# Kernel optimization log

Hardware: AMD Instinct MI355X
Metric: run time of the kernel (lower is better)

## Reference

```python
import jax, jax.numpy as jnp
from jax import lax
import numpy as np

N, T, PD, TD, F, E, GB = 2048, 256, 5, 5, 128, 65536, 5


def _lstm_layer(x, Wih, Whh, bih, bhh):
    # x: [B, T, D] -> [B, T, H], torch LSTM gate order (i, f, g, o)
    B = x.shape[0]
    H = Whh.shape[1]
    b = bih + bhh

    def step(carry, xt):
        h, c = carry
        gates = xt @ Wih.T + h @ Whh.T + b
        i, f, g, o = jnp.split(gates, 4, axis=-1)
        c = jax.nn.sigmoid(f) * c + jax.nn.sigmoid(i) * jnp.tanh(g)
        h = jax.nn.sigmoid(o) * jnp.tanh(c)
        return (h, c), h

    h0 = jnp.zeros((B, H), x.dtype)
    _, hs = lax.scan(step, (h0, h0), jnp.swapaxes(x, 0, 1))
    return jnp.swapaxes(hs, 0, 1)


def _attention(x, W1, b1, W2, b2):
    # Fused prefix (cumulative causal) softmax attention.
    # Original loops over t computing softmax(scores[:, :t+1]); here:
    # ctx[t] = cumsum(e * x)[t] / cumsum(e)[t] with a global max shift
    # (softmax is shift-invariant, so this equals the per-prefix softmax).
    s = (jnp.tanh(x @ W1.T + b1) @ W2.T + b2)[..., 0]  # [B, T]
    e = jnp.exp(s - jnp.max(s, axis=1, keepdims=True))  # [B, T]
    num = jnp.cumsum(e[..., None] * x, axis=1)          # [B, T, D]
    den = jnp.cumsum(e, axis=1)[..., None]              # [B, T, 1]
    return jnp.sum(num / den, axis=1)                   # [B, D]


def _gcn(x, W, b, edge_index, edge_weight):
    # PyG GCNConv with normalize=True: add self-loops (w=1), symmetric norm.
    n = x.shape[0]
    loop = jnp.arange(n)
    row = jnp.concatenate([edge_index[0], loop])
    col = jnp.concatenate([edge_index[1], loop])
    w = jnp.concatenate([edge_weight, jnp.ones((n,), edge_weight.dtype)])
    deg = jax.ops.segment_sum(w, col, num_segments=n)
    dinv = jnp.where(deg > 0, deg ** -0.5, 0.0)
    norm = dinv[row] * w * dinv[col]
    h = x @ W.T
    out = jax.ops.segment_sum(norm[:, None] * h[row], col, num_segments=n)
    return out + b


def _forward(price, global_trend, p_weights, t_weights,
             lp_Wih0, lp_Whh0, lp_bih0, lp_bhh0, lp_Wih1, lp_Whh1, lp_bih1, lp_bhh1,
             lt_Wih0, lt_Whh0, lt_bih0, lt_bhh0, lt_Wih1, lt_Whh1, lt_bih1, lt_bhh1,
             ap_W1, ap_b1, ap_W2, ap_b2, at_W1, at_b1, at_W2, at_b2,
             gp1_W, gp1_b, gp2_W, gp2_b, gt1_W, gt1_b, gt2_W, gt2_b,
             mlp_W, mlp_b, p_edge_index, t_edge_index):
    x = _lstm_layer(price, lp_Wih0, lp_Whh0, lp_bih0, lp_bhh0)
    x = _lstm_layer(x, lp_Wih1, lp_Whh1, lp_bih1, lp_bhh1)
    x = _attention(x, ap_W1, ap_b1, ap_W2, ap_b2)            # [N, F]
    g = _lstm_layer(global_trend, lt_Wih0, lt_Whh0, lt_bih0, lt_bhh0)
    g = _lstm_layer(g, lt_Wih1, lt_Whh1, lt_bih1, lt_bhh1)
    g = _attention(g, at_W1, at_b1, at_W2, at_b2)            # [GB, F]
    pg = _gcn(x, gp1_W, gp1_b, p_edge_index, p_weights)
    pg = _gcn(pg, gp2_W, gp2_b, p_edge_index, p_weights)     # [N, F]
    # NOTE: original feeds x (not g) into the trend graph convs.
    tg = _gcn(x, gt1_W, gt1_b, t_edge_index, t_weights)
    tg = _gcn(tg, gt2_W, gt2_b, t_edge_index, t_weights)     # [N, F]
    trend = tg @ g.T                                         # [N, GB]
    feat = jnp.concatenate([pg, trend], axis=1)              # [N, F+GB]
    return jax.nn.sigmoid(feat @ mlp_W.T + mlp_b)            # [N, 1]


def setup_inputs() -> dict:
    key = jax.random.key(0)
    ks = iter(jax.random.split(key, 64))
    nrm = lambda shape, s=0.05: jax.random.normal(next(ks), shape, jnp.float32) * s
    inp = {}
    inp['price'] = jax.random.normal(next(ks), (N, T, PD), jnp.float32)
    inp['global_trend'] = jax.random.normal(next(ks), (GB, T, TD), jnp.float32)
    inp['p_edge_index'] = jax.random.randint(next(ks), (2, E), 0, N)
    inp['p_weights'] = jax.random.uniform(next(ks), (E,), jnp.float32)
    inp['t_edge_index'] = jax.random.randint(next(ks), (2, E), 0, N)
    inp['t_weights'] = jax.random.uniform(next(ks), (E,), jnp.float32)
    for pre, d in (('lp', PD), ('lt', TD)):
        inp[pre + '_Wih0'] = nrm((4 * F, d)); inp[pre + '_Whh0'] = nrm((4 * F, F))
        inp[pre + '_bih0'] = nrm((4 * F,));   inp[pre + '_bhh0'] = nrm((4 * F,))
        inp[pre + '_Wih1'] = nrm((4 * F, F)); inp[pre + '_Whh1'] = nrm((4 * F, F))
        inp[pre + '_bih1'] = nrm((4 * F,));   inp[pre + '_bhh1'] = nrm((4 * F,))
    for pre in ('ap', 'at'):
        inp[pre + '_W1'] = nrm((F, F)); inp[pre + '_b1'] = jnp.zeros((F,), jnp.float32)
        inp[pre + '_W2'] = nrm((1, F)); inp[pre + '_b2'] = jnp.zeros((1,), jnp.float32)
    for pre in ('gp', 'gt'):
        inp[pre + '1_W'] = nrm((16, F)); inp[pre + '1_b'] = jnp.zeros((16,), jnp.float32)
        inp[pre + '2_W'] = nrm((F, 16)); inp[pre + '2_b'] = jnp.zeros((F,), jnp.float32)
    inp['mlp_W'] = nrm((1, F + GB)); inp['mlp_b'] = jnp.zeros((1,), jnp.float32)
    return inp


def reference(price, global_trend, p_edge_index, p_weights, t_edge_index, t_weights,
              lp_Wih0, lp_Whh0, lp_bih0, lp_bhh0, lp_Wih1, lp_Whh1, lp_bih1, lp_bhh1,
              lt_Wih0, lt_Whh0, lt_bih0, lt_bhh0, lt_Wih1, lt_Whh1, lt_bih1, lt_bhh1,
              ap_W1, ap_b1, ap_W2, ap_b2, at_W1, at_b1, at_W2, at_b2,
              gp1_W, gp1_b, gp2_W, gp2_b, gt1_W, gt1_b, gt2_W, gt2_b,
              mlp_W, mlp_b):
    return _forward(price, global_trend, p_weights, t_weights,
                    lp_Wih0, lp_Whh0, lp_bih0, lp_bhh0, lp_Wih1, lp_Whh1, lp_bih1, lp_bhh1,
                    lt_Wih0, lt_Whh0, lt_bih0, lt_bhh0, lt_Wih1, lt_Whh1, lt_bih1, lt_bhh1,
                    ap_W1, ap_b1, ap_W2, ap_b2, at_W1, at_b1, at_W2, at_b2,
                    gp1_W, gp1_b, gp2_W, gp2_b, gt1_W, gt1_b, gt2_W, gt2_b,
                    mlp_W, mlp_b, p_edge_index, t_edge_index)
```

## Files before the change

### kernel.cpp

```cpp
#include <hip/hip_runtime.h>
#include <hip/hip_bf16.h>
#include <cstddef>

#define TT    256
#define NROW  2048
#define GBN   5
#define EDG   65536

using f32x4  = __attribute__((ext_vector_type(4))) float;
using bf16x8 = __attribute__((ext_vector_type(8))) short;

__device__ __forceinline__ void pinv(bf16x8& x) { asm volatile("" : "+v"(x)); }

__device__ __forceinline__ void barrier_lgkm() {
  asm volatile("s_waitcnt lgkmcnt(0)" ::: "memory");
  __builtin_amdgcn_s_barrier();
}

__device__ __forceinline__ float exp2fa(float x) { float r; asm("v_exp_f32 %0, %1" : "=v"(r) : "v"(x)); return r; }
__device__ __forceinline__ float rcpfa(float x)  { float r; asm("v_rcp_f32 %0, %1" : "=v"(r) : "v"(x)); return r; }
#define L2E 1.4426950408889634f
__device__ __forceinline__ float sigf(float x) { return rcpfa(1.0f + exp2fa(x * -L2E)); }
__device__ __forceinline__ float tanh_fast(float x) {
  float t = exp2fa(x * (-2.0f * L2E));
  return (1.0f - t) * rcpfa(1.0f + t);
}

enum : int {
  XBUF   = 425984,
  GBUFO  = 688128,
  DINVP  = 688768,
  DINVT  = 690816,
  H16    = 692864,
  PG1    = 725632,
  H128   = 758400,
  PGB    = 1020544,
  TG1    = 1282688,
  TGB    = 1315456,
  WS_END = 1577600
};

enum : int {
  N_P0   = 0,
  N_P1I  = 65536,
  N_P1H  = 131072,
  N_PA   = 196608,
  N_T0   = 212992,
  N_T1I  = 278528,
  N_T1H  = 344064,
  N_TA   = 409600
};

enum : long long {
  C0S_O   = 1577600,
  C1S_O   = 1841792,
  H1IMG_O = 2105984,
  SMST_O  = 2370176,
  NUMS_O  = 2374304,
  ACCOS_O = 2638496,
  H0S_O   = 2902688
};

struct SmemPipe {
  ushort a[2][2048];
  ushort b[2][2048];
  float  x[2560];
  float  s[2][8][16];
};

__global__ void k_pack(const float* __restrict__ Wa, const float* __restrict__ Wb,
                       int K1, int K2, int NT, int KS, ushort* __restrict__ dst) {
  int t = blockIdx.x * blockDim.x + threadIdx.x;
  int total = KS * NT * 2 * 64;
  if (t >= total) return;
  int lane = t & 63;
  int part = (t >> 6) & 1;
  int rest = t >> 7;
  int nt = rest % NT, kk = rest / NT;
  int j = nt * 16 + (lane & 15);
  int kbase = kk * 32 + (lane >> 4) * 8;
  bf16x8 o;
  #pragma unroll
  for (int e = 0; e < 8; ++e) {
    int k = kbase + e;
    float x = (k < K1) ? Wa[(size_t)j * K1 + k] : Wb[(size_t)j * K2 + (k - K1)];
    __hip_bfloat16 hi = __float2bfloat16(x);
    ushort u;
    if (part == 0) {
      u = *(ushort*)&hi;
    } else {
      float lo = x - __bfloat162float(hi);
      __hip_bfloat16 lob = __float2bfloat16(lo);
      u = *(ushort*)&lob;
    }
    o[e] = (short)u;
  }
  ((bf16x8*)dst)[t] = o;
}

__global__ void k_zero(float* __restrict__ p, int n) {
  int i = blockIdx.x * blockDim.x + threadIdx.x;
  if (i < n) p[i] = 0.0f;
}
__global__ void k_fill1(float* __restrict__ p, int n) {
  int i = blockIdx.x * blockDim.x + threadIdx.x;
  if (i < n) p[i] = 1.0f;
}
__global__ void k_deg(const int* __restrict__ col, const float* __restrict__ w,
                      float* __restrict__ deg, int n) {
  int i = blockIdx.x * blockDim.x + threadIdx.x;
  if (i < n) atomicAdd(&deg[col[i]], w[i]);
}
__global__ void k_dinv(float* __restrict__ deg, int n) {
  int i = blockIdx.x * blockDim.x + threadIdx.x;
  if (i < n) deg[i] = rsqrtf(deg[i]);
}

__device__ static void lstm0_body(
    SmemPipe* sm, int b,
    const float* __restrict__ price, const float* __restrict__ gtrend,
    const float* __restrict__ ws_ro, ushort* __restrict__ h0S, float* __restrict__ c0S,
    const float* __restrict__ Wih0p, const float* __restrict__ bi0p, const float* __restrict__ bh0p,
    const float* __restrict__ Wih0t, const float* __restrict__ bi0t, const float* __restrict__ bh0t,
    int nPrice, int t0, int TCp, int first)
{
  const int tid = threadIdx.x;
  const int w = tid >> 6, l = tid & 63;
  const int lq = l >> 4, lr = l & 15;
  const int rb = lq * 4;
  const int kcol = w * 16 + lr;
  const bool isP = b < nPrice;
  const int R = isP ? 16 : GBN;
  const float* seq = isP ? (price + (size_t)b * 16 * (TT * 5)) : gtrend;
  const ushort* S0 = (const ushort*)(ws_ro + (isP ? N_P0 : N_T0));
  const float* Wih0 = isP ? Wih0p : Wih0t;
  const float* bi0 = isP ? bi0p : bi0t;
  const float* bh0 = isP ? bh0p : bh0t;

  auto h0hi = sm->a;
  auto h0lo = sm->b;
  float* xsa = sm->x;

  bf16x8 wh[4][4], wl[4][4];
  #pragma unroll
  for (int kk = 0; kk < 4; ++kk)
    #pragma unroll
    for (int g = 0; g < 4; ++g) {
      int blk = (kk * 32 + (w + 8 * g)) * 2;
      wh[kk][g] = ((const bf16x8*)S0)[(blk + 0) * 64 + l];
      wl[kk][g] = ((const bf16x8*)S0)[(blk + 1) * 64 + l];
      pinv(wh[kk][g]); pinv(wl[kk][g]);
    }
  float wih0r[4][5], bg0[4];
  #pragma unroll
  for (int g = 0; g < 4; ++g) {
    int j = kcol + 128 * g;
    bg0[g] = bi0[j] + bh0[j];
    #pragma unroll
    for (int k = 0; k < 5; ++k) wih0r[g][k] = Wih0[j * 5 + k];
  }

  const size_t bstr = (size_t)b * (size_t)TCp * 4096;
  float c0[4] = {0, 0, 0, 0};

  for (int i = tid; i < TCp * 80; i += 512) {
    int tl = i / 80, rem = i % 80, r = rem / 5, k = rem % 5;
    xsa[tl * 80 + rem] = (r < R) ? seq[(size_t)r * (TT * 5) + (size_t)(t0 + tl) * 5 + k] : 0.0f;
  }
  if (first) {
    for (int i = tid; i < 2048; i += 512) { h0hi[0][i] = 0; h0lo[0][i] = 0; }
  } else {
    const size_t lb = bstr + (size_t)(TCp - 1) * 4096;
    *(uint2*)&h0hi[0][4 * tid] = *(const uint2*)&h0S[lb + 4 * tid];
    *(uint2*)&h0lo[0][4 * tid] = *(const uint2*)&h0S[lb + 2048 + 4 * tid];
    #pragma unroll
    for (int reg = 0; reg < 4; ++reg)
      c0[reg] = c0S[(size_t)b * 2048 + (size_t)(rb + reg) * 128 + kcol];
  }
  __syncthreads();

  const int kkhi = (kcol >> 3) & 3;
  const int eo = kcol & 7;
  const int b0w = rb + 16 * kkhi;
  const int kkw = kcol >> 5;
  int wro[4];
  #pragma unroll
  for (int reg = 0; reg < 4; ++reg) wro[reg] = kkw * 512 + (b0w + (reg ^ lq)) * 8 + eo;
  const int rdo = (l ^ ((l >> 2) & 3)) * 8;

  int cur = 0;
  for (int tl = 0; tl < TCp; ++tl) {
    const int nxt = cur ^ 1;
    if (tl > 0) {
      *(uint2*)&h0S[bstr + (size_t)(tl - 1) * 4096 + 4 * tid] = *(const uint2*)&h0hi[cur][4 * tid];
      *(uint2*)&h0S[bstr + (size_t)(tl - 1) * 4096 + 2048 + 4 * tid] = *(const uint2*)&h0lo[cur][4 * tid];
    }

    f32x4 acc[4];
    #pragma unroll
    for (int g = 0; g < 4; ++g) acc[g] = (f32x4){bg0[g], bg0[g], bg0[g], bg0[g]};
    #pragma unroll
    for (int k = 0; k < 5; ++k) {
      float xv[4];
      #pragma unroll
      for (int reg = 0; reg < 4; ++reg) xv[reg] = xsa[tl * 80 + (rb + reg) * 5 + k];
      #pragma unroll
      for (int g = 0; g < 4; ++g)
        #pragma unroll
        for (int reg = 0; reg < 4; ++reg)
          acc[g][reg] = fmaf(xv[reg], wih0r[g][k], acc[g][reg]);
    }
    #pragma unroll
    for (int kk = 0; kk < 4; ++kk) {
      bf16x8 ah = *(const bf16x8*)&h0hi[cur][kk * 512 + rdo];
      bf16x8 al = *(const bf16x8*)&h0lo[cur][kk * 512 + rdo];
      #pragma unroll
      for (int g = 0; g < 4; ++g) {
        acc[g] = __builtin_amdgcn_mfma_f32_16x16x32_bf16(ah, wh[kk][g], acc[g], 0, 0, 0);
        acc[g] = __builtin_amdgcn_mfma_f32_16x16x32_bf16(al, wh[kk][g], acc[g], 0, 0, 0);
        acc[g] = __builtin_amdgcn_mfma_f32_16x16x32_bf16(ah, wl[kk][g], acc[g], 0, 0, 0);
      }
    }
    #pragma unroll
    for (int reg = 0; reg < 4; ++reg) {
      float gi = acc[0][reg], gf = acc[1][reg], gg = acc[2][reg], go = acc[3][reg];
      float c = sigf(gf) * c0[reg] + sigf(gi) * tanh_fast(gg);
      c0[reg] = c;
      float h = sigf(go) * tanh_fast(c);
      __hip_bfloat16 hb = __float2bfloat16(h);
      float lo = h - __bfloat162float(hb);
      __hip_bfloat16 lb = __float2bfloat16(lo);
      h0hi[nxt][wro[reg]] = *(ushort*)&hb;
      h0lo[nxt][wro[reg]] = *(ushort*)&lb;
    }
    barrier_lgkm();
    cur = nxt;
  }
  *(uint2*)&h0S[bstr + (size_t)(TCp - 1) * 4096 + 4 * tid] = *(const uint2*)&h0hi[cur][4 * tid];
  *(uint2*)&h0S[bstr + (size_t)(TCp - 1) * 4096 + 2048 + 4 * tid] = *(const uint2*)&h0lo[cur][4 * tid];

  #pragma unroll
  for (int reg = 0; reg < 4; ++reg)
    c0S[(size_t)b * 2048 + (size_t)(rb + reg) * 128 + kcol] = c0[reg];
}

__device__ static void lstm1_body(
    SmemPipe* sm, int b,
    const float* __restrict__ pre1, const float* __restrict__ ws_ro,
    float* __restrict__ xout, float* __restrict__ gout,
    float* __restrict__ c1S, ushort* __restrict__ h1imgS, float* __restrict__ smS,
    float* __restrict__ numS, float* __restrict__ accOS,
    const float* __restrict__ apB1, const float* __restrict__ apW2, const float* __restrict__ apB2,
    const float* __restrict__ atB1, const float* __restrict__ atW2, const float* __restrict__ atB2,
    int nPrice, int TCp, int first)
{
  const int tid = threadIdx.x;
  const int w = tid >> 6, l = tid & 63;
  const int lq = l >> 4, lr = l & 15;
  const int rb = lq * 4;
  const int kcol = w * 16 + lr;
  const bool isP = b < nPrice;
  const int R = isP ? 16 : GBN;
  const ushort* S1H = (const ushort*)(ws_ro + (isP ? N_P1H : N_T1H));
  const ushort* SA  = (const ushort*)(ws_ro + (isP ? N_PA : N_TA));
  const float* b1ap = isP ? apB1 : atB1;
  const float* w2p  = isP ? apW2 : atW2;
  const float  b2v  = isP ? apB2[0] : atB2[0];

  auto h1hi = sm->a;
  auto h1lo = sm->b;
  auto sbuf = sm->s;

  bf16x8 hh[4][4], hl[4][4];
  #pragma unroll
  for (int kk = 0; kk < 4; ++kk)
    #pragma unroll
    for (int g = 0; g < 4; ++g) {
      int blk = (kk * 32 + (w + 8 * g)) * 2;
      hh[kk][g] = ((const bf16x8*)S1H)[(blk + 0) * 64 + l];
      hl[kk][g] = ((const bf16x8*)S1H)[(blk + 1) * 64 + l];
      pinv(hh[kk][g]); pinv(hl[kk][g]);
    }
  bf16x8 wa[4], wal[4];
  #pragma unroll
  for (int kk = 0; kk < 4; ++kk) {
    wa[kk]  = ((const bf16x8*)SA)[((kk * 8 + w) * 2 + 0) * 64 + l];
    wal[kk] = ((const bf16x8*)SA)[((kk * 8 + w) * 2 + 1) * 64 + l];
    pinv(wa[kk]); pinv(wal[kk]);
  }
  const float w2r = w2p[kcol], b1ar = b1ap[kcol];

  float c1[4] = {0, 0, 0, 0}, h1r[4] = {0, 0, 0, 0}, h1r_prev[4];
  float num[4] = {0, 0, 0, 0}, accO[4] = {0, 0, 0, 0};
  float m_run[4], den_r[4];

  if (first) {
    for (int i = tid; i < 2048; i += 512) { h1hi[0][i] = 0; h1lo[0][i] = 0; }
    #pragma unroll
    for (int reg = 0; reg < 4; ++reg) { m_run[reg] = -1e30f; den_r[reg] = 0.0f; }
  } else {
    const size_t ib = (size_t)b * 4096;
    *(uint2*)&h1hi[0][4 * tid] = *(const uint2*)&h1imgS[ib + 4 * tid];
    *(uint2*)&h1lo[0][4 * tid] = *(const uint2*)&h1imgS[ib + 2048 + 4 * tid];
    const size_t sb = (size_t)b * 2048;
    #pragma unroll
    for (int reg = 0; reg < 4; ++reg) {
      size_t o = sb + (size_t)(rb + reg) * 128 + kcol;
      c1[reg] = c1S[o];
      num[reg] = numS[o];
      accO[reg] = accOS[o];
      m_run[reg] = smS[(size_t)b * 32 + (size_t)(rb + reg) * 2];
      den_r[reg] = smS[(size_t)b * 32 + (size_t)(rb + reg) * 2 + 1];
    }
  }
  __syncthreads();

  const int kkhi = (kcol >> 3) & 3;
  const int eo = kcol & 7;
  const int b0w = rb + 16 * kkhi;
  const int kkw = kcol >> 5;
  int wro[4];
  #pragma unroll
  for (int reg = 0; reg < 4; ++reg) wro[reg] = kkw * 512 + (b0w + (reg ^ lq)) * 8 + eo;
  const int rdo = (l ^ ((l >> 2) & 3)) * 8;

  const float* pbase = pre1 + (size_t)b * TCp * 8192 + (size_t)tid * 16;

  f32x4 pnext[4];
  #pragma unroll
  for (int g = 0; g < 4; ++g) pnext[g] = *(const f32x4*)&pbase[g * 4];

  int cur = 0;
  for (int tl = 0; tl < TCp; ++tl) {
    const int nxt = cur ^ 1;
    f32x4 acc[4];
    #pragma unroll
    for (int g = 0; g < 4; ++g) acc[g] = pnext[g];
    if (tl + 1 < TCp) {
      #pragma unroll
      for (int g = 0; g < 4; ++g)
        pnext[g] = *(const f32x4*)&pbase[(size_t)(tl + 1) * 8192 + g * 4];
    }

    #pragma unroll
    for (int kk = 0; kk < 4; ++kk) {
      bf16x8 ah = *(const bf16x8*)&h1hi[cur][kk * 512 + rdo];
      bf16x8 al = *(const bf16x8*)&h1lo[cur][kk * 512 + rdo];
      #pragma unroll
      for (int g = 0; g < 4; ++g) {
        acc[g] = __builtin_amdgcn_mfma_f32_16x16x32_bf16(ah, hh[kk][g], acc[g], 0, 0, 0);
        acc[g] = __builtin_amdgcn_mfma_f32_16x16x32_bf16(al, hh[kk][g], acc[g], 0, 0, 0);
        acc[g] = __builtin_amdgcn_mfma_f32_16x16x32_bf16(ah, hl[kk][g], acc[g], 0, 0, 0);
      }
    }
    #pragma unroll
    for (int reg = 0; reg < 4; ++reg) {
      h1r_prev[reg] = h1r[reg];
      float gi = acc[0][reg], gf = acc[1][reg], gg = acc[2][reg], go = acc[3][reg];
      float c = sigf(gf) * c1[reg] + sigf(gi) * tanh_fast(gg);
      c1[reg] = c;
      float h = sigf(go) * tanh_fast(c);
      h1r[reg] = h;
      __hip_bfloat16 hb = __float2bfloat16(h);
      float lo = h - __bfloat162float(hb);
      __hip_bfloat16 lb = __float2bfloat16(lo);
      h1hi[nxt][wro[reg]] = *(ushort*)&hb;
      h1lo[nxt][wro[reg]] = *(ushort*)&lb;
    }
    barrier_lgkm();

    if (tl > 0) {
      const int pb = (tl - 1) & 1;
      #pragma unroll
      for (int reg = 0; reg < 4; ++reg) {
        float s = b2v;
        #pragma unroll
        for (int ww = 0; ww < 8; ++ww) s += sbuf[pb][ww][rb + reg];
        float m0 = m_run[reg];
        float nm = fmaxf(m0, s);
        float e = exp2fa((s - nm) * L2E), sc = exp2fa((m0 - nm) * L2E);
        float d = den_r[reg] * sc + e;
        m_run[reg] = nm; den_r[reg] = d;
        num[reg] = num[reg] * sc + e * h1r_prev[reg];
        accO[reg] = fmaf(num[reg], rcpfa(d), accO[reg]);
      }
    }

    f32x4 aa = (f32x4){b1ar, b1ar, b1ar, b1ar};
    #pragma unroll
    for (int kk = 0; kk < 4; ++kk) {
      bf16x8 ah = *(const bf16x8*)&h1hi[nxt][kk * 512 + rdo];
      bf16x8 al = *(const bf16x8*)&h1lo[nxt][kk * 512 + rdo];
      aa = __builtin_amdgcn_mfma_f32_16x16x32_bf16(ah, wa[kk], aa, 0, 0, 0);
      aa = __builtin_amdgcn_mfma_f32_16x16x32_bf16(al, wa[kk], aa, 0, 0, 0);
      aa = __builtin_amdgcn_mfma_f32_16x16x32_bf16(ah, wal[kk], aa, 0, 0, 0);
    }
    float p[4];
    #pragma unroll
    for (int reg = 0; reg < 4; ++reg) p[reg] = tanh_fast(aa[reg]) * w2r;
    #pragma unroll
    for (int m = 1; m < 16; m <<= 1) {
      #pragma unroll
      for (int reg = 0; reg < 4; ++reg) p[reg] += __shfl_xor(p[reg], m);
    }
    if (lr == 0) {
      #pragma unroll
      for (int reg = 0; reg < 4; ++reg) sbuf[tl & 1][w][rb + reg] = p[reg];
    }
    cur = nxt;
  }
  barrier_lgkm();
  {
    const int pb = (TCp - 1) & 1;
    #pragma unroll
    for (int reg = 0; reg < 4; ++reg) {
      float s = b2v;
      #pragma unroll
      for (int ww = 0; ww < 8; ++ww) s += sbuf[pb][ww][rb + reg];
      float m0 = m_run[reg];
      float nm = fmaxf(m0, s);
      float e = exp2fa((s - nm) * L2E), sc = exp2fa((m0 - nm) * L2E);
      float d = den_r[reg] * sc + e;
      m_run[reg] = nm; den_r[reg] = d;
      num[reg] = num[reg] * sc + e * h1r[reg];
      accO[reg] = fmaf(num[reg], rcpfa(d), accO[reg]);
    }
  }

  {
    const size_t ib = (size_t)b * 4096;
    *(uint2*)&h1imgS[ib + 4 * tid] = *(const uint2*)&h1hi[cur][4 * tid];
    *(uint2*)&h1imgS[ib + 2048 + 4 * tid] = *(const uint2*)&h1lo[cur][4 * tid];
    const size_t sb = (size_t)b * 2048;
    #pragma unroll
    for (int reg = 0; reg < 4; ++reg) {
      size_t o = sb + (size_t)(rb + reg) * 128 + kcol;
      c1S[o] = c1[reg];
      numS[o] = num[reg];
      accOS[o] = accO[reg];
    }
    if (w == 0 && lr == 0) {
      #pragma unroll
      for (int reg = 0; reg < 4; ++reg) {
        smS[(size_t)b * 32 + (size_t)(rb + reg) * 2] = m_run[reg];
        smS[(size_t)b * 32 + (size_t)(rb + reg) * 2 + 1] = den_r[reg];
      }
    }
  }

  float* dstx = isP ? (xout + (size_t)b * 16 * 128) : gout;
  #pragma unroll
  for (int reg = 0; reg < 4; ++reg) {
    int r = rb + reg;
    if (r < R) dstx[(size_t)r * 128 + kcol] = accO[reg];
  }
}

__global__ __launch_bounds__(512, 2) void k_pipe(
    const float* __restrict__ price, const float* __restrict__ gtrend,
    const float* __restrict__ ws_ro, ushort* __restrict__ h0S, float* __restrict__ c0S,
    const float* __restrict__ Wih0p, const float* __restrict__ bi0p, const float* __restrict__ bh0p,
    const float* __restrict__ Wih0t, const float* __restrict__ bi0t, const float* __restrict__ bh0t,
    const float* __restrict__ pre1,
    float* __restrict__ xout, float* __restrict__ gout,
    float* __restrict__ c1S, ushort* __restrict__ h1imgS, float* __restrict__ smS,
    float* __restrict__ numS, float* __restrict__ accOS,
    const float* __restrict__ apB1, const float* __restrict__ apW2, const float* __restrict__ apB2,
    const float* __restrict__ atB1, const float* __restrict__ atW2, const float* __restrict__ atB2,
    int nPrice, int t0A, int TCp, int firstA, int firstB, int doA, int doB)
{
  __shared__ SmemPipe sm;
  const int bid = blockIdx.x;
  if (bid < 129) {
    if (doA)
      lstm0_body(&sm, bid, price, gtrend, ws_ro, h0S, c0S,
                 Wih0p, bi0p, bh0p, Wih0t, bi0t, bh0t, nPrice, t0A, TCp, firstA);
  } else {
    if (doB)
      lstm1_body(&sm, bid - 129, pre1, ws_ro, xout, gout,
                 c1S, h1imgS, smS, numS, accOS,
                 apB1, apW2, apB2, atB1, atW2, atB2, nPrice, TCp, firstB);
  }
}

__global__ __launch_bounds__(512, 2) void k_pre1(
    const ushort* __restrict__ h0S, const float* __restrict__ ws_ro,
    float* __restrict__ pre1,
    const float* __restrict__ bi1p, const float* __restrict__ bh1p,
    const float* __restrict__ bi1t, const float* __restrict__ bh1t,
    int nPrice, int TCp, int nsub)
{
  const int b = blockIdx.x / nsub, sub = blockIdx.x % nsub;
  const int tid = threadIdx.x;
  const int w = tid >> 6, l = tid & 63;
  const int lr = l & 15;
  const int kcol = w * 16 + lr;
  const bool isP = b < nPrice;
  const ushort* S1I = (const ushort*)(ws_ro + (isP ? N_P1I : N_T1I));
  const float* bi1 = isP ? bi1p : bi1t;
  const float* bh1 = isP ? bh1p : bh1t;
  float bg1[4];
  #pragma unroll
  for (int g = 0; g < 4; ++g) bg1[g] = bi1[kcol + 128 * g] + bh1[kcol + 128 * g];
  const int rdo = (l ^ ((l >> 2) & 3)) * 8;
  const size_t bstr = (size_t)b * (size_t)TCp * 4096;
  const int t0 = sub * 4;

  f32x4 acc[4][4];
  #pragma unroll
  for (int ts = 0; ts < 4; ++ts)
    #pragma unroll
    for (int g = 0; g < 4; ++g) acc[ts][g] = (f32x4){bg1[g], bg1[g], bg1[g], bg1[g]};

  #pragma unroll
  for (int kk = 0; kk < 4; ++kk) {
    bf16x8 bh_[4], bl_[4];
    #pragma unroll
    for (int g = 0; g < 4; ++g) {
      int blk = (kk * 32 + (w + 8 * g)) * 2;
      bh_[g] = ((const bf16x8*)S1I)[(blk + 0) * 64 + l];
      bl_[g] = ((const bf16x8*)S1I)[(blk + 1) * 64 + l];
    }
    #pragma unroll
    for (int ts = 0; ts < 4; ++ts) {
      const size_t tb = bstr + (size_t)(t0 + ts) * 4096 + kk * 512 + rdo;
      bf16x8 ah = *(const bf16x8*)&h0S[tb];
      bf16x8 al = *(const bf16x8*)&h0S[tb + 2048];
      #pragma unroll
      for (int g = 0; g < 4; ++g) {
        acc[ts][g] = __builtin_amdgcn_mfma_f32_16x16x32_bf16(ah, bh_[g], acc[ts][g], 0, 0, 0);
        acc[ts][g] = __builtin_amdgcn_mfma_f32_16x16x32_bf16(al, bh_[g], acc[ts][g], 0, 0, 0);
        acc[ts][g] = __builtin_amdgcn_mfma_f32_16x16x32_bf16(ah, bl_[g], acc[ts][g], 0, 0, 0);
      }
    }
  }
  #pragma unroll
  for (int ts = 0; ts < 4; ++ts)
    #pragma unroll
    for (int g = 0; g < 4; ++g)
      *(f32x4*)&pre1[((size_t)b * TCp + (t0 + ts)) * 8192 + (size_t)tid * 16 + g * 4] = acc[ts][g];
}

__global__ void k_lin(const float* __restrict__ x, const float* __restrict__ W,
                      float* __restrict__ h, int M, int K, int n) {
  int i = blockIdx.x * blockDim.x + threadIdx.x;
  if (i >= n) return;
  int r = i / M, m = i % M;
  const float* xr = x + (size_t)r * K;
  const float* wm = W + (size_t)m * K;
  float a = 0.f;
  for (int k = 0; k < K; ++k) a = fmaf(xr[k], wm[k], a);
  h[i] = a;
}

__global__ void k_scatter(const int* __restrict__ rowi, const int* __restrict__ coli,
                          const float* __restrict__ w, const float* __restrict__ dinv,
                          const float* __restrict__ h, float* __restrict__ outp,
                          int M, long long n) {
  long long i = (long long)blockIdx.x * blockDim.x + threadIdx.x;
  if (i >= n) return;
  int e = (int)(i / M), f = (int)(i % M);
  int rs = rowi[e], cd = coli[e];
  float nrm = dinv[rs] * w[e] * dinv[cd];
  atomicAdd(&outp[(size_t)cd * M + f], nrm * h[(size_t)rs * M + f]);
}

__global__ void k_gcn_fin(float* __restrict__ io, const float* __restrict__ h,
                          const float* __restrict__ dinv, const float* __restrict__ b,
                          int M, int n) {
  int i = blockIdx.x * blockDim.x + threadIdx.x;
  if (i >= n) return;
  int v = i / M, f = i % M;
  float dv = dinv[v];
  io[i] += dv * dv * h[i] + b[f];
}

__global__ __launch_bounds__(256) void k_final(const float* __restrict__ pg, const float* __restrict__ tg,
                                               const float* __restrict__ g, const float* __restrict__ mw,
                                               const float* __restrict__ mb, float* __restrict__ outp) {
  int wv = threadIdx.x >> 6, ln = threadIdx.x & 63;
  int r = blockIdx.x * 4 + wv;
  const float* pr = pg + (size_t)r * 128;
  const float* tr = tg + (size_t)r * 128;
  float pa = pr[ln] * mw[ln] + pr[ln + 64] * mw[ln + 64];
  float t0 = tr[ln], t1 = tr[ln + 64];
  float s[GBN];
  #pragma unroll
  for (int gb = 0; gb < GBN; ++gb)
    s[gb] = g[gb * 128 + ln] * t0 + g[gb * 128 + 64 + ln] * t1;
  #pragma unroll
  for (int o = 32; o > 0; o >>= 1) {
    pa += __shfl_down(pa, o);
    #pragma unroll
    for (int gb = 0; gb < GBN; ++gb) s[gb] += __shfl_down(s[gb], o);
  }
  if (ln == 0) {
    float lg = pa + mb[0];
    #pragma unroll
    for (int gb = 0; gb < GBN; ++gb) lg = fmaf(s[gb], mw[128 + gb], lg);
    outp[r] = 1.0f / (1.0f + __expf(-lg));
  }
}

static inline int gdiv(long long n) { return (int)((n + 255) / 256); }

extern "C" void kernel_launch(void* const* d_in, const int* in_sizes, int n_in,
                              void* d_out, int out_size, void* d_ws, size_t ws_size,
                              hipStream_t stream) {
  const float* price  = (const float*)d_in[0];
  const float* gtrend = (const float*)d_in[1];
  const int*   p_ei   = (const int*)d_in[2];
  const float* p_w    = (const float*)d_in[3];
  const int*   t_ei   = (const int*)d_in[4];
  const float* t_w    = (const float*)d_in[5];
  const float* lpWih0 = (const float*)d_in[6];
  const float* lpWhh0 = (const float*)d_in[7];
  const float* lpBih0 = (const float*)d_in[8];
  const float* lpBhh0 = (const float*)d_in[9];
  const float* lpWih1 = (const float*)d_in[10];
  const float* lpWhh1 = (const float*)d_in[11];
  const float* lpBih1 = (const float*)d_in[12];
  const float* lpBhh1 = (const float*)d_in[13];
  const float* ltWih0 = (const float*)d_in[14];
  const float* ltWhh0 = (const float*)d_in[15];
  const float* ltBih0 = (const float*)d_in[16];
  const float* ltBhh0 = (const float*)d_in[17];
  const float* ltWih1 = (const float*)d_in[18];
  const float* ltWhh1 = (const float*)d_in[19];
  const float* ltBih1 = (const float*)d_in[20];
  const float* ltBhh1 = (const float*)d_in[21];
  const float* apW1 = (const float*)d_in[22];
  const float* apB1 = (const float*)d_in[23];
  const float* apW2 = (const float*)d_in[24];
  const float* apB2 = (const float*)d_in[25];
  const float* atW1 = (const float*)d_in[26];
  const float* atB1 = (const float*)d_in[27];
  const float* atW2 = (const float*)d_in[28];
  const float* atB2 = (const float*)d_in[29];
  const float* gp1W = (const float*)d_in[30];
  const float* gp1b = (const float*)d_in[31];
  const float* gp2W = (const float*)d_in[32];
  const float* gp2b = (const float*)d_in[33];
  const float* gt1W = (const float*)d_in[34];
  const float* gt1b = (const float*)d_in[35];
  const float* gt2W = (const float*)d_in[36];
  const float* gt2b = (const float*)d_in[37];
  const float* mlpW = (const float*)d_in[38];
  const float* mlpb = (const float*)d_in[39];

  float* ws = (float*)d_ws;
  float* outp = (float*)d_out;
  if (ws_size < (size_t)WS_END * sizeof(float)) return;

  int TC = 0;
  for (int cand = 32; cand >= 8; cand >>= 1) {
    unsigned long long need = ((unsigned long long)H0S_O + 129ULL * cand * (2048ULL + 8192ULL)) * 4ULL;
    if ((unsigned long long)ws_size >= need) { TC = cand; break; }
  }
  if (TC == 0) return;

  k_pack<<<gdiv(16384), 256, 0, stream>>>(lpWhh0, lpWhh0, 128, 128, 32, 4, (ushort*)(ws + N_P0));
  k_pack<<<gdiv(16384), 256, 0, stream>>>(lpWih1, lpWih1, 128, 128, 32, 4, (ushort*)(ws + N_P1I));
  k_pack<<<gdiv(16384), 256, 0, stream>>>(lpWhh1, lpWhh1, 128, 128, 32, 4, (ushort*)(ws + N_P1H));
  k_pack<<<gdiv(4096),  256, 0, stream>>>(apW1,   apW1,   128, 128,  8, 4, (ushort*)(ws + N_PA));
  k_pack<<<gdiv(16384), 256, 0, stream>>>(ltWhh0, ltWhh0, 128, 128, 32, 4, (ushort*)(ws + N_T0));
  k_pack<<<gdiv(16384), 256, 0, stream>>>(ltWih1, ltWih1, 128, 128, 32, 4, (ushort*)(ws + N_T1I));
  k_pack<<<gdiv(16384), 256, 0, stream>>>(ltWhh1, ltWhh1, 128, 128, 32, 4, (ushort*)(ws + N_T1H));
  k_pack<<<gdiv(4096),  256, 0, stream>>>(atW1,   atW1,   128, 128,  8, 4, (ushort*)(ws + N_TA));

  k_fill1<<<gdiv(NROW), 256, 0, stream>>>(ws + DINVP, NROW);
  k_deg<<<gdiv(EDG), 256, 0, stream>>>(p_ei + EDG, p_w, ws + DINVP, EDG);
  k_dinv<<<gdiv(NROW), 256, 0, stream>>>(ws + DINVP, NROW);
  k_fill1<<<gdiv(NROW), 256, 0, stream>>>(ws + DINVT, NROW);
  k_deg<<<gdiv(EDG), 256, 0, stream>>>(t_ei + EDG, t_w, ws + DINVT, EDG);
  k_dinv<<<gdiv(NROW), 256, 0, stream>>>(ws + DINVT, NROW);

  ushort* h0S = (ushort*)(ws + H0S_O);
  float*  pre1 = ws + H0S_O + (long long)129 * TC * 2048;
  {
    const int CH = TT / TC;
    const int nsub = TC / 4;
    for (int c = 0; c < CH; ++c) {
      k_pipe<<<258, 512, 0, stream>>>(price, gtrend, ws, h0S, ws + C0S_O,
                                      lpWih0, lpBih0, lpBhh0,
                                      ltWih0, ltBih0, ltBhh0,
                                      pre1, ws + XBUF, ws + GBUFO,
                                      ws + C1S_O, (ushort*)(ws + H1IMG_O), ws + SMST_O,
                                      ws + NUMS_O, ws + ACCOS_O,
                                      apB1, apW2, apB2, atB1, atW2, atB2,
                                      128, c * TC, TC,
                                      c == 0 ? 1 : 0,
                                      c == 1 ? 1 : 0,
                                      1, c > 0 ? 1 : 0);
      k_pre1<<<129 * nsub, 512, 0, stream>>>(h0S, ws, pre1,
                                             lpBih1, lpBhh1, ltBih1, ltBhh1,
                                             128, TC, nsub);
    }
    k_pipe<<<258, 512, 0, stream>>>(price, gtrend, ws, h0S, ws + C0S_O,
                                    lpWih0, lpBih0, lpBhh0,
                                    ltWih0, ltBih0, ltBhh0,
                                    pre1, ws + XBUF, ws + GBUFO,
                                    ws + C1S_O, (ushort*)(ws + H1IMG_O), ws + SMST_O,
                                    ws + NUMS_O, ws + ACCOS_O,
                                    apB1, apW2, apB2, atB1, atW2, atB2,
                                    128, 0, TC,
                                    0, CH == 1 ? 1 : 0,
                                    0, 1);
  }

  k_lin<<<gdiv(NROW * 16), 256, 0, stream>>>(ws + XBUF, gp1W, ws + H16, 16, 128, NROW * 16);
  k_zero<<<gdiv(NROW * 16), 256, 0, stream>>>(ws + PG1, NROW * 16);
  k_scatter<<<gdiv((long long)EDG * 16), 256, 0, stream>>>(p_ei, p_ei + EDG, p_w, ws + DINVP,
                                                           ws + H16, ws + PG1, 16, (long long)EDG * 16);
  k_gcn_fin<<<gdiv(NROW * 16), 256, 0, stream>>>(ws + PG1, ws + H16, ws + DINVP, gp1b, 16, NROW * 16);
  k_lin<<<gdiv(NROW * 128), 256, 0, stream>>>(ws + PG1, gp2W, ws + H128, 128, 16, NROW * 128);
  k_zero<<<gdiv(NROW * 128), 256, 0, stream>>>(ws + PGB, NROW * 128);
  k_scatter<<<gdiv((long long)EDG * 128), 256, 0, stream>>>(p_ei, p_ei + EDG, p_w, ws + DINVP,
                                                            ws + H128, ws + PGB, 128, (long long)EDG * 128);
  k_gcn_fin<<<gdiv(NROW * 128), 256, 0, stream>>>(ws + PGB, ws + H128, ws + DINVP, gp2b, 128, NROW * 128);

  k_lin<<<gdiv(NROW * 16), 256, 0, stream>>>(ws + XBUF, gt1W, ws + H16, 16, 128, NROW * 16);
  k_zero<<<gdiv(NROW * 16), 256, 0, stream>>>(ws + TG1, NROW * 16);
  k_scatter<<<gdiv((long long)EDG * 16), 256, 0, stream>>>(t_ei, t_ei + EDG, t_w, ws + DINVT,
                                                           ws + H16, ws + TG1, 16, (long long)EDG * 16);
  k_gcn_fin<<<gdiv(NROW * 16), 256, 0, stream>>>(ws + TG1, ws + H16, ws + DINVT, gt1b, 16, NROW * 16);
  k_lin<<<gdiv(NROW * 128), 256, 0, stream>>>(ws + TG1, gt2W, ws + H128, 128, 16, NROW * 128);
  k_zero<<<gdiv(NROW * 128), 256, 0, stream>>>(ws + TGB, NROW * 128);
  k_scatter<<<gdiv((long long)EDG * 128), 256, 0, stream>>>(t_ei, t_ei + EDG, t_w, ws + DINVT,
                                                            ws + H128, ws + TGB, 128, (long long)EDG * 128);
  k_gcn_fin<<<gdiv(NROW * 128), 256, 0, stream>>>(ws + TGB, ws + H128, ws + DINVT, gt2b, 128, NROW * 128);

  k_final<<<512, 256, 0, stream>>>(ws + PGB, ws + TGB, ws + GBUFO, mlpW, mlpb, outp);
}
```

Baseline: 2.367 ms.

## Process 32 rows per layer-0 LSTM block to fit pipeline grid on CUs

Each layer-0 LSTM block now carries two 16-row MFMA tiles, so 32 price rows instead of 16. That halves the layer-0 block count and shrinks the k_pipe grid from 258 to 194 blocks. The h0 staging layout, the c0 state layout and the workspace offsets are resized to match, and k_pre1 maps its 16-row tiles onto the new 32-row layout. Shared memory is padded, apparently so each block has a CU to itself and no CU has to share between two blocks, which the 258-block grid forced. The cost is twice the per-step MFMA and activation work inside each layer-0 block, which may lengthen the serial recurrence step.

```diff
diff --git a/kernel.cpp b/kernel.cpp
--- a/kernel.cpp
+++ b/kernel.cpp
@@ -53,19 +53,20 @@
 
 enum : long long {
   C0S_O   = 1577600,
-  C1S_O   = 1841792,
-  H1IMG_O = 2105984,
-  SMST_O  = 2370176,
-  NUMS_O  = 2374304,
-  ACCOS_O = 2638496,
-  H0S_O   = 2902688
+  C1S_O   = 1843840,
+  H1IMG_O = 2108032,
+  SMST_O  = 2372224,
+  NUMS_O  = 2376352,
+  ACCOS_O = 2640544,
+  H0S_O   = 2904736
 };
 
-struct SmemPipe {
-  ushort a[2][2048];
-  ushort b[2][2048];
-  float  x[2560];
+struct __align__(16) SmemPipe {
+  ushort a[2][4096];
+  ushort b[2][4096];
+  float  x[5120];
   float  s[2][8][16];
+  float  pad[8192];
 };
 
 __global__ void k_pack(const float* __restrict__ Wa, const float* __restrict__ Wb,
@@ -122,16 +123,16 @@
     const float* __restrict__ ws_ro, ushort* __restrict__ h0S, float* __restrict__ c0S,
     const float* __restrict__ Wih0p, const float* __restrict__ bi0p, const float* __restrict__ bh0p,
     const float* __restrict__ Wih0t, const float* __restrict__ bi0t, const float* __restrict__ bh0t,
-    int nPrice, int t0, int TCp, int first)
+    int nP32, int t0, int TCp, int first)
 {
   const int tid = threadIdx.x;
   const int w = tid >> 6, l = tid & 63;
   const int lq = l >> 4, lr = l & 15;
   const int rb = lq * 4;
   const int kcol = w * 16 + lr;
-  const bool isP = b < nPrice;
-  const int R = isP ? 16 : GBN;
-  const float* seq = isP ? (price + (size_t)b * 16 * (TT * 5)) : gtrend;
+  const bool isP = b < nP32;
+  const int R = isP ? 32 : GBN;
+  const float* seq = isP ? (price + (size_t)b * 32 * (TT * 5)) : gtrend;
   const ushort* S0 = (const ushort*)(ws_ro + (isP ? N_P0 : N_T0));
   const float* Wih0 = isP ? Wih0p : Wih0t;
   const float* bi0 = isP ? bi0p : bi0t;
@@ -160,22 +161,24 @@
     for (int k = 0; k < 5; ++k) wih0r[g][k] = Wih0[j * 5 + k];
   }
 
-  const size_t bstr = (size_t)b * (size_t)TCp * 4096;
-  float c0[4] = {0, 0, 0, 0};
-
-  for (int i = tid; i < TCp * 80; i += 512) {
-    int tl = i / 80, rem = i % 80, r = rem / 5, k = rem % 5;
-    xsa[tl * 80 + rem] = (r < R) ? seq[(size_t)r * (TT * 5) + (size_t)(t0 + tl) * 5 + k] : 0.0f;
+  const size_t bstr = (size_t)b * (size_t)TCp * 8192;
+  float c0[2][4] = {{0, 0, 0, 0}, {0, 0, 0, 0}};
+
+  for (int i = tid; i < TCp * 160; i += 512) {
+    int tl = i / 160, rem = i % 160, r = rem / 5, k = rem % 5;
+    xsa[tl * 160 + rem] = (r < R) ? seq[(size_t)r * (TT * 5) + (size_t)(t0 + tl) * 5 + k] : 0.0f;
   }
   if (first) {
-    for (int i = tid; i < 2048; i += 512) { h0hi[0][i] = 0; h0lo[0][i] = 0; }
+    for (int i = tid; i < 4096; i += 512) { h0hi[0][i] = 0; h0lo[0][i] = 0; }
   } else {
-    const size_t lb = bstr + (size_t)(TCp - 1) * 4096;
-    *(uint2*)&h0hi[0][4 * tid] = *(const uint2*)&h0S[lb + 4 * tid];
-    *(uint2*)&h0lo[0][4 * tid] = *(const uint2*)&h0S[lb + 2048 + 4 * tid];
-    #pragma unroll
-    for (int reg = 0; reg < 4; ++reg)
-      c0[reg] = c0S[(size_t)b * 2048 + (size_t)(rb + reg) * 128 + kcol];
+    const size_t lb = bstr + (size_t)(TCp - 1) * 8192;
+    *(uint4*)&h0hi[0][8 * tid] = *(const uint4*)&h0S[lb + 8 * tid];
+    *(uint4*)&h0lo[0][8 * tid] = *(const uint4*)&h0S[lb + 4096 + 8 * tid];
+    #pragma unroll
+    for (int t = 0; t < 2; ++t)
+      #pragma unroll
+      for (int reg = 0; reg < 4; ++reg)
+        c0[t][reg] = c0S[(size_t)b * 4096 + (size_t)(t * 16 + rb + reg) * 128 + kcol];
   }
   __syncthreads();
 
@@ -192,56 +195,72 @@
   for (int tl = 0; tl < TCp; ++tl) {
     const int nxt = cur ^ 1;
     if (tl > 0) {
-      *(uint2*)&h0S[bstr + (size_t)(tl - 1) * 4096 + 4 * tid] = *(const uint2*)&h0hi[cur][4 * tid];
-      *(uint2*)&h0S[bstr + (size_t)(tl - 1) * 4096 + 2048 + 4 * tid] = *(const uint2*)&h0lo[cur][4 * tid];
-    }
-
-    f32x4 acc[4];
-    #pragma unroll
-    for (int g = 0; g < 4; ++g) acc[g] = (f32x4){bg0[g], bg0[g], bg0[g], bg0[g]};
+      *(uint4*)&h0S[bstr + (size_t)(tl - 1) * 8192 + 8 * tid] = *(const uint4*)&h0hi[cur][8 * tid];
+      *(uint4*)&h0S[bstr + (size_t)(tl - 1) * 8192 + 4096 + 8 * tid] = *(const uint4*)&h0lo[cur][8 * tid];
+    }
+
+    f32x4 acc[2][4];
+    #pragma unroll
+    for (int t = 0; t < 2; ++t)
+      #pragma unroll
+      for (int g = 0; g < 4; ++g) acc[t][g] = (f32x4){bg0[g], bg0[g], bg0[g], bg0[g]};
     #pragma unroll
     for (int k = 0; k < 5; ++k) {
-      float xv[4];
-      #pragma unroll
-      for (int reg = 0; reg < 4; ++reg) xv[reg] = xsa[tl * 80 + (rb + reg) * 5 + k];
-      #pragma unroll
-      for (int g = 0; g < 4; ++g)
+      float xv[2][4];
+      #pragma unroll
+      for (int t = 0; t < 2; ++t)
         #pragma unroll
         for (int reg = 0; reg < 4; ++reg)
-          acc[g][reg] = fmaf(xv[reg], wih0r[g][k], acc[g][reg]);
+          xv[t][reg] = xsa[tl * 160 + (t * 16 + rb + reg) * 5 + k];
+      #pragma unroll
+      for (int t = 0; t < 2; ++t)
+        #pragma unroll
+        for (int g = 0; g < 4; ++g)
+          #pragma unroll
+          for (int reg = 0; reg < 4; ++reg)
+            acc[t][g][reg] = fmaf(xv[t][reg], wih0r[g][k], acc[t][g][reg]);
     }
     #pragma unroll
     for (int kk = 0; kk < 4; ++kk) {
-      bf16x8 ah = *(const bf16x8*)&h0hi[cur][kk * 512 + rdo];
-      bf16x8 al = *(const bf16x8*)&h0lo[cur][kk * 512 + rdo];
+      bf16x8 ah0 = *(const bf16x8*)&h0hi[cur][kk * 512 + rdo];
+      bf16x8 al0 = *(const bf16x8*)&h0lo[cur][kk * 512 + rdo];
+      bf16x8 ah1 = *(const bf16x8*)&h0hi[cur][2048 + kk * 512 + rdo];
+      bf16x8 al1 = *(const bf16x8*)&h0lo[cur][2048 + kk * 512 + rdo];
       #pragma unroll
       for (int g = 0; g < 4; ++g) {
-        acc[g] = __builtin_amdgcn_mfma_f32_16x16x32_bf16(ah, wh[kk][g], acc[g], 0, 0, 0);
-        acc[g] = __builtin_amdgcn_mfma_f32_16x16x32_bf16(al, wh[kk][g], acc[g], 0, 0, 0);
-        acc[g] = __builtin_amdgcn_mfma_f32_16x16x32_bf16(ah, wl[kk][g], acc[g], 0, 0, 0);
+        acc[0][g] = __builtin_amdgcn_mfma_f32_16x16x32_bf16(ah0, wh[kk][g], acc[0][g], 0, 0, 0);
+        acc[0][g] = __builtin_amdgcn_mfma_f32_16x16x32_bf16(al0, wh[kk][g], acc[0][g], 0, 0, 0);
+        acc[0][g] = __builtin_amdgcn_mfma_f32_16x16x32_bf16(ah0, wl[kk][g], acc[0][g], 0, 0, 0);
+        acc[1][g] = __builtin_amdgcn_mfma_f32_16x16x32_bf16(ah1, wh[kk][g], acc[1][g], 0, 0, 0);
+        acc[1][g] = __builtin_amdgcn_mfma_f32_16x16x32_bf16(al1, wh[kk][g], acc[1][g], 0, 0, 0);
+        acc[1][g] = __builtin_amdgcn_mfma_f32_16x16x32_bf16(ah1, wl[kk][g], acc[1][g], 0, 0, 0);
       }
     }
     #pragma unroll
-    for (int reg = 0; reg < 4; ++reg) {
-      float gi = acc[0][reg], gf = acc[1][reg], gg = acc[2][reg], go = acc[3][reg];
-      float c = sigf(gf) * c0[reg] + sigf(gi) * tanh_fast(gg);
-      c0[reg] = c;
-      float h = sigf(go) * tanh_fast(c);
-      __hip_bfloat16 hb = __float2bfloat16(h);
-      float lo = h - __bfloat162float(hb);
-      __hip_bfloat16 lb = __float2bfloat16(lo);
-      h0hi[nxt][wro[reg]] = *(ushort*)&hb;
-      h0lo[nxt][wro[reg]] = *(ushort*)&lb;
-    }
+    for (int t = 0; t < 2; ++t)
+      #pragma unroll
+      for (int reg = 0; reg < 4; ++reg) {
+        float gi = acc[0 + t][0][reg], gf = acc[t][1][reg], gg = acc[t][2][reg], go = acc[t][3][reg];
+        float c = sigf(gf) * c0[t][reg] + sigf(gi) * tanh_fast(gg);
+        c0[t][reg] = c;
+        float h = sigf(go) * tanh_fast(c);
+        __hip_bfloat16 hb = __float2bfloat16(h);
+        float lo = h - __bfloat162float(hb);
+        __hip_bfloat16 lb = __float2bfloat16(lo);
+        h0hi[nxt][t * 2048 + wro[reg]] = *(ushort*)&hb;
+        h0lo[nxt][t * 2048 + wro[reg]] = *(ushort*)&lb;
+      }
     barrier_lgkm();
     cur = nxt;
   }
-  *(uint2*)&h0S[bstr + (size_t)(TCp - 1) * 4096 + 4 * tid] = *(const uint2*)&h0hi[cur][4 * tid];
-  *(uint2*)&h0S[bstr + (size_t)(TCp - 1) * 4096 + 2048 + 4 * tid] = *(const uint2*)&h0lo[cur][4 * tid];
-
-  #pragma unroll
-  for (int reg = 0; reg < 4; ++reg)
-    c0S[(size_t)b * 2048 + (size_t)(rb + reg) * 128 + kcol] = c0[reg];
+  *(uint4*)&h0S[bstr + (size_t)(TCp - 1) * 8192 + 8 * tid] = *(const uint4*)&h0hi[cur][8 * tid];
+  *(uint4*)&h0S[bstr + (size_t)(TCp - 1) * 8192 + 4096 + 8 * tid] = *(const uint4*)&h0lo[cur][8 * tid];
+
+  #pragma unroll
+  for (int t = 0; t < 2; ++t)
+    #pragma unroll
+    for (int reg = 0; reg < 4; ++reg)
+      c0S[(size_t)b * 4096 + (size_t)(t * 16 + rb + reg) * 128 + kcol] = c0[t][reg];
 }
 
 __device__ static void lstm1_body(
@@ -467,19 +486,19 @@
     float* __restrict__ numS, float* __restrict__ accOS,
     const float* __restrict__ apB1, const float* __restrict__ apW2, const float* __restrict__ apB2,
     const float* __restrict__ atB1, const float* __restrict__ atW2, const float* __restrict__ atB2,
-    int nPrice, int t0A, int TCp, int firstA, int firstB, int doA, int doB)
+    int t0A, int TCp, int firstA, int firstB, int doA, int doB)
 {
   __shared__ SmemPipe sm;
   const int bid = blockIdx.x;
-  if (bid < 129) {
+  if (bid < 65) {
     if (doA)
       lstm0_body(&sm, bid, price, gtrend, ws_ro, h0S, c0S,
-                 Wih0p, bi0p, bh0p, Wih0t, bi0t, bh0t, nPrice, t0A, TCp, firstA);
+                 Wih0p, bi0p, bh0p, Wih0t, bi0t, bh0t, 64, t0A, TCp, firstA);
   } else {
     if (doB)
-      lstm1_body(&sm, bid - 129, pre1, ws_ro, xout, gout,
+      lstm1_body(&sm, bid - 65, pre1, ws_ro, xout, gout,
                  c1S, h1imgS, smS, numS, accOS,
-                 apB1, apW2, apB2, atB1, atW2, atB2, nPrice, TCp, firstB);
+                 apB1, apW2, apB2, atB1, atW2, atB2, 128, TCp, firstB);
   }
 }
 
@@ -490,12 +509,13 @@
     const float* __restrict__ bi1t, const float* __restrict__ bh1t,
     int nPrice, int TCp, int nsub)
 {
-  const int b = blockIdx.x / nsub, sub = blockIdx.x % nsub;
+  const int b16 = blockIdx.x / nsub, sub = blockIdx.x % nsub;
+  const int b32 = b16 >> 1, tile = b16 & 1;
   const int tid = threadIdx.x;
   const int w = tid >> 6, l = tid & 63;
   const int lr = l & 15;
   const int kcol = w * 16 + lr;
-  const bool isP = b < nPrice;
+  const bool isP = b16 < nPrice;
   const ushort* S1I = (const ushort*)(ws_ro + (isP ? N_P1I : N_T1I));
   const float* bi1 = isP ? bi1p : bi1t;
   const float* bh1 = isP ? bh1p : bh1t;
@@ -503,7 +523,7 @@
   #pragma unroll
   for (int g = 0; g < 4; ++g) bg1[g] = bi1[kcol + 128 * g] + bh1[kcol + 128 * g];
   const int rdo = (l ^ ((l >> 2) & 3)) * 8;
-  const size_t bstr = (size_t)b * (size_t)TCp * 4096;
+  const size_t bstr = (size_t)b32 * (size_t)TCp * 8192;
   const int t0 = sub * 4;
 
   f32x4 acc[4][4];
@@ -523,9 +543,9 @@
     }
     #pragma unroll
     for (int ts = 0; ts < 4; ++ts) {
-      const size_t tb = bstr + (size_t)(t0 + ts) * 4096 + kk * 512 + rdo;
+      const size_t tb = bstr + (size_t)(t0 + ts) * 8192 + tile * 2048 + kk * 512 + rdo;
       bf16x8 ah = *(const bf16x8*)&h0S[tb];
-      bf16x8 al = *(const bf16x8*)&h0S[tb + 2048];
+      bf16x8 al = *(const bf16x8*)&h0S[tb + 4096];
       #pragma unroll
       for (int g = 0; g < 4; ++g) {
         acc[ts][g] = __builtin_amdgcn_mfma_f32_16x16x32_bf16(ah, bh_[g], acc[ts][g], 0, 0, 0);
@@ -538,7 +558,7 @@
   for (int ts = 0; ts < 4; ++ts)
     #pragma unroll
     for (int g = 0; g < 4; ++g)
-      *(f32x4*)&pre1[((size_t)b * TCp + (t0 + ts)) * 8192 + (size_t)tid * 16 + g * 4] = acc[ts][g];
+      *(f32x4*)&pre1[((size_t)b16 * TCp + (t0 + ts)) * 8192 + (size_t)tid * 16 + g * 4] = acc[ts][g];
 }
 
 __global__ void k_lin(const float* __restrict__ x, const float* __restrict__ W,
@@ -654,7 +674,8 @@
 
   int TC = 0;
   for (int cand = 32; cand >= 8; cand >>= 1) {
-    unsigned long long need = ((unsigned long long)H0S_O + 129ULL * cand * (2048ULL + 8192ULL)) * 4ULL;
+    unsigned long long need = ((unsigned long long)H0S_O +
+                               65ULL * cand * 4096ULL + 129ULL * cand * 8192ULL) * 4ULL;
     if ((unsigned long long)ws_size >= need) { TC = cand; break; }
   }
   if (TC == 0) return;
@@ -676,36 +697,33 @@
   k_dinv<<<gdiv(NROW), 256, 0, stream>>>(ws + DINVT, NROW);
 
   ushort* h0S = (ushort*)(ws + H0S_O);
-  float*  pre1 = ws + H0S_O + (long long)129 * TC * 2048;
+  float*  pre1 = ws + H0S_O + (long long)65 * TC * 4096;
   {
     const int CH = TT / TC;
     const int nsub = TC / 4;
     for (int c = 0; c < CH; ++c) {
-      k_pipe<<<258, 512, 0, stream>>>(price, gtrend, ws, h0S, ws + C0S_O,
+      k_pipe<<<194, 512, 0, stream>>>(price, gtrend, ws, h0S, ws + C0S_O,
                                       lpWih0, lpBih0, lpBhh0,
                                       ltWih0, ltBih0, ltBhh0,
                                       pre1, ws + XBUF, ws + GBUFO,
                                       ws + C1S_O, (ushort*)(ws + H1IMG_O), ws + SMST_O,
                                       ws + NUMS_O, ws + ACCOS_O,
                                       apB1, apW2, apB2, atB1, atW2, atB2,
-                                      128, c * TC, TC,
-                                      c == 0 ? 1 : 0,
-                                      c == 1 ? 1 : 0,
+                                      c * TC, TC,
+                                      c == 0 ? 1 : 0, c == 1 ? 1 : 0,
                                       1, c > 0 ? 1 : 0);
       k_pre1<<<129 * nsub, 512, 0, stream>>>(h0S, ws, pre1,
                                              lpBih1, lpBhh1, ltBih1, ltBhh1,
                                              128, TC, nsub);
     }
-    k_pipe<<<258, 512, 0, stream>>>(price, gtrend, ws, h0S, ws + C0S_O,
+    k_pipe<<<194, 512, 0, stream>>>(price, gtrend, ws, h0S, ws + C0S_O,
                                     lpWih0, lpBih0, lpBhh0,
                                     ltWih0, ltBih0, ltBhh0,
                                     pre1, ws + XBUF, ws + GBUFO,
                                     ws + C1S_O, (ushort*)(ws + H1IMG_O), ws + SMST_O,
                                     ws + NUMS_O, ws + ACCOS_O,
                                     apB1, apW2, apB2, atB1, atW2, atB2,
-                                    128, 0, TC,
-                                    0, CH == 1 ? 1 : 0,
-                                    0, 1);
+                                    0, TC, 0, CH == 1 ? 1 : 0, 0, 1);
   }
 
   k_lin<<<gdiv(NROW * 16), 256, 0, stream>>>(ws + XBUF, gp1W, ws + H16, 16, 128, NROW * 16);
```

Result: slower. 2.426 ms (+2.5%).
